# Optimization experiments

Hardware: AMD Instinct MI355X
Metric: run time of the kernel (lower is better)

The kernel has to match this reference:

```python
import jax, jax.numpy as jnp
import numpy as np

N = 50000
E = 600000


def gcn_conv(x, W, b, src, dst, n):
    # PyG GCNConv: h = x @ W; add self-loops; symmetric normalization; aggregate; + bias
    h = x @ W  # [N, out]
    deg = jnp.zeros((n,), h.dtype).at[dst].add(1.0) + 1.0  # self-loop included
    dinv = jax.lax.rsqrt(deg)  # deg >= 1, always finite
    coef = dinv[src] * dinv[dst]  # [E]
    msg = h[src] * coef[:, None]  # [E, out]  (the memory-bound gather)
    agg = jax.ops.segment_sum(msg, dst, num_segments=n)
    agg = agg + h * (dinv * dinv)[:, None]  # self-loop contribution
    return agg + b


def setup_inputs() -> dict:
    key = jax.random.key(0)
    ks = jax.random.split(key, 8)
    x = jax.random.normal(ks[0], (N, 128), dtype=jnp.float32)
    edge_index = jax.random.randint(ks[1], (2, E), 0, N, dtype=jnp.int64 if jax.config.jax_enable_x64 else jnp.int32)
    def glorot(k, fan_in, fan_out):
        s = jnp.sqrt(6.0 / (fan_in + fan_out))
        return jax.random.uniform(k, (fan_in, fan_out), jnp.float32, -s, s)
    W1 = glorot(ks[2], 128, 128)
    b1 = jnp.zeros((128,), jnp.float32)
    W2 = glorot(ks[3], 128, 64)
    b2 = jnp.zeros((64,), jnp.float32)
    W3 = glorot(ks[4], 64, 16)
    b3 = jnp.zeros((16,), jnp.float32)
    return {"x": x, "edge_index": edge_index, "W1": W1, "b1": b1, "W2": W2, "b2": b2, "W3": W3, "b3": b3}


def reference(x, edge_index, W1, b1, W2, b2, W3, b3):
    src, dst = edge_index[0], edge_index[1]
    n = x.shape[0]
    h = jax.nn.relu(gcn_conv(x, W1, b1, src, dst, n))
    h = jax.nn.relu(gcn_conv(h, W2, b2, src, dst, n))
    h = gcn_conv(h, W3, b3, src, dst, n)
    return h
```

## Files before the change

### kernel.cpp

```cpp
#include <hip/hip_runtime.h>
#include <hip/hip_fp16.h>
#include <type_traits>


typedef _Float16 f16x8 __attribute__((ext_vector_type(8)));
typedef float f32x4 __attribute__((ext_vector_type(4)));

#define CSR_CAP 64

__device__ inline float2 h2f(unsigned int u) {
  __half2 h = __builtin_bit_cast(__half2, u);
  return __half22float2(h);
}

__device__ inline void fma8h(float4& a0, float4& a1, const uint4& g, float w) {
  float2 f0 = h2f(g.x), f1 = h2f(g.y), f2 = h2f(g.z), f3 = h2f(g.w);
  a0.x = fmaf(f0.x, w, a0.x);
  a0.y = fmaf(f0.y, w, a0.y);
  a0.z = fmaf(f1.x, w, a0.z);
  a0.w = fmaf(f1.y, w, a0.w);
  a1.x = fmaf(f2.x, w, a1.x);
  a1.y = fmaf(f2.y, w, a1.y);
  a1.z = fmaf(f3.x, w, a1.z);
  a1.w = fmaf(f3.y, w, a1.w);
}

__device__ inline unsigned int pack2h(float x, float y) {
  __half2 h = __floats2half2_rn(x, y);
  return __builtin_bit_cast(unsigned int, h);
}

__device__ inline uint2 pack4h(const float4& v) {
  uint2 r;
  r.x = pack2h(v.x, v.y);
  r.y = pack2h(v.z, v.w);
  return r;
}

template <int K, int F, typename TIN>
__global__ __launch_bounds__(256) void gemm_mfma(const TIN* __restrict__ A,
                                                 const float* __restrict__ W,
                                                 __half* __restrict__ C16, int n,
                                                 int nwaves, int ngemm,
                                                 const int* __restrict__ src,
                                                 const int* __restrict__ dst,
                                                 int* __restrict__ cur,
                                                 int* __restrict__ csr, int E) {
  constexpr int KP = K + 8;
  constexpr int KS = K / 32;
  constexpr int NT = F / 16;

  if (blockIdx.x >= ngemm) {
    int e = (blockIdx.x - ngemm) * 256 + threadIdx.x;
    if (e < E) {
      int d = dst[e];
      int pos = atomicAdd(&cur[d], 1);
      if (pos >= CSR_CAP) pos = CSR_CAP - 1;
      csr[(size_t)d * CSR_CAP + pos] = src[e];
    }
    return;
  }

  __shared__ __half Ws[F * KP];

  int t = threadIdx.x;
  for (int i = t; i < K * F; i += 256) {
    int kk = i / F, nn = i % F;
    Ws[nn * KP + kk] = __float2half(W[i]);
  }
  __syncthreads();

  int wave = blockIdx.x * 4 + (t >> 6);
  if (wave >= nwaves) return;
  int lane = t & 63;
  int m = lane & 15;
  int quad = lane >> 4;

  int arow = wave * 16 + m;
  if (arow >= n) arow = n - 1;

  f16x8 af[KS];
  if constexpr (std::is_same_v<TIN, float>) {
#pragma unroll
    for (int ks = 0; ks < KS; ++ks) {
      const float* p = A + (size_t)arow * K + ks * 32 + quad * 8;
      float4 lo = *(const float4*)p;
      float4 hi = *(const float4*)(p + 4);
      f16x8 a;
      a[0] = (_Float16)lo.x; a[1] = (_Float16)lo.y;
      a[2] = (_Float16)lo.z; a[3] = (_Float16)lo.w;
      a[4] = (_Float16)hi.x; a[5] = (_Float16)hi.y;
      a[6] = (_Float16)hi.z; a[7] = (_Float16)hi.w;
      af[ks] = a;
    }
  } else {
#pragma unroll
    for (int ks = 0; ks < KS; ++ks)
      af[ks] = *(const f16x8*)(const void*)&A[(size_t)arow * K + ks * 32 + quad * 8];
  }

  f32x4 acc[NT];
#pragma unroll
  for (int nt = 0; nt < NT; ++nt) acc[nt] = (f32x4){0.f, 0.f, 0.f, 0.f};
#pragma unroll
  for (int nt = 0; nt < NT; ++nt)
#pragma unroll
    for (int ks = 0; ks < KS; ++ks) {
      f16x8 b = *(const f16x8*)(const void*)&Ws[(nt * 16 + m) * KP + ks * 32 + quad * 8];
      acc[nt] = __builtin_amdgcn_mfma_f32_16x16x32_f16(af[ks], b, acc[nt], 0, 0, 0);
    }

  int rbase = wave * 16 + quad * 4;
#pragma unroll
  for (int nt = 0; nt < NT; ++nt)
#pragma unroll
    for (int r = 0; r < 4; ++r) {
      int rr = rbase + r;
      if (rr < n) C16[(size_t)rr * F + nt * 16 + m] = __float2half(acc[nt][r]);
    }
}

template <int K, int F, int CPL, int EU>
__global__ __launch_bounds__(512) void aggmm(
    const __half* __restrict__ hprev, const float* __restrict__ W,
    const float* __restrict__ bias, const int* __restrict__ cnt,
    const int* __restrict__ csr, __half* __restrict__ C16, int n) {
  constexpr int KP = K + 8;
  constexpr int KS = K / 32;
  constexpr int NT = F / 16;
  constexpr int TPN = 8;
  constexpr int RS = K / 8;
  static_assert(TPN * CPL == RS, "chunk coverage");

  __shared__ __half Ws[F * KP];
  __shared__ __half As[64 * KP];

  int t = threadIdx.x;
  for (int i = t; i < K * F; i += 512) {
    int kk = i / F, nn = i % F;
    Ws[nn * KP + kk] = __float2half(W[i]);
  }

  int wid = t >> 6;
  int lane = t & 63;
  int nb = blockIdx.x * 64;

  {
    int sub = lane / TPN;
    int fl = lane % TPN;
    int nib = wid * 8 + sub;
    int node = nb + nib;
    int nd = node < n ? node : n - 1;
    const uint4* h4 = (const uint4*)hprev;
    int c0 = cnt[nd];
    float di = rsqrtf((float)c0 + 1.0f);
    float sc = di * di;
    int cc = c0 < CSR_CAP ? c0 : CSR_CAP;
    float4 acc[CPL][2];
#pragma unroll
    for (int c = 0; c < CPL; ++c) {
      acc[c][0] = make_float4(0.f, 0.f, 0.f, 0.f);
      acc[c][1] = make_float4(0.f, 0.f, 0.f, 0.f);
    }
#pragma unroll
    for (int c = 0; c < CPL; ++c) {
      uint4 sv = h4[(size_t)nd * RS + fl + c * TPN];
      fma8h(acc[c][0], acc[c][1], sv, sc);
    }
    int j = nd * CSR_CAP;
    int e = j + cc;
    int p[EU];
#pragma unroll
    for (int u = 0; u < EU; ++u) p[u] = csr[j + u];
    for (; j + EU <= e;) {
      uint4 g[EU][CPL];
#pragma unroll
      for (int u = 0; u < EU; ++u)
#pragma unroll
        for (int c = 0; c < CPL; ++c) g[u][c] = h4[(size_t)p[u] * RS + fl + c * TPN];
      int cs[EU];
#pragma unroll
      for (int u = 0; u < EU; ++u) cs[u] = cnt[p[u]];
      j += EU;
      int pn[EU];
#pragma unroll
      for (int u = 0; u < EU; ++u) pn[u] = csr[j + u];
#pragma unroll
      for (int u = 0; u < EU; ++u) {
        float w = rsqrtf((float)cs[u] + 1.0f) * di;
#pragma unroll
        for (int c = 0; c < CPL; ++c) fma8h(acc[c][0], acc[c][1], g[u][c], w);
      }
#pragma unroll
      for (int u = 0; u < EU; ++u) p[u] = pn[u];
    }
#pragma unroll
    for (int u = 0; u < EU; ++u) {
      if (j + u < e) {
        float w = rsqrtf((float)cnt[p[u]] + 1.0f) * di;
#pragma unroll
        for (int c = 0; c < CPL; ++c) {
          uint4 g = h4[(size_t)p[u] * RS + fl + c * TPN];
          fma8h(acc[c][0], acc[c][1], g, w);
        }
      }
    }
#pragma unroll
    for (int c = 0; c < CPL; ++c) {
      int ch = fl + c * TPN;
      float4 b0 = *(const float4*)&bias[ch * 8];
      float4 b1 = *(const float4*)&bias[ch * 8 + 4];
      float4 r0 = make_float4(fmaxf(acc[c][0].x + b0.x, 0.f), fmaxf(acc[c][0].y + b0.y, 0.f),
                              fmaxf(acc[c][0].z + b0.z, 0.f), fmaxf(acc[c][0].w + b0.w, 0.f));
      float4 r1 = make_float4(fmaxf(acc[c][1].x + b1.x, 0.f), fmaxf(acc[c][1].y + b1.y, 0.f),
                              fmaxf(acc[c][1].z + b1.z, 0.f), fmaxf(acc[c][1].w + b1.w, 0.f));
      uint2 lo = pack4h(r0), hi = pack4h(r1);
      uint4 pk;
      pk.x = lo.x; pk.y = lo.y; pk.z = hi.x; pk.w = hi.y;
      *(uint4*)&As[(size_t)nib * KP + ch * 8] = pk;
    }
  }

  __syncthreads();

  if (wid < 4) {
    int m = lane & 15;
    int quad = lane >> 4;
    const __half* At = &As[(size_t)wid * 16 * KP];
    f16x8 af[KS];
#pragma unroll
    for (int ks = 0; ks < KS; ++ks)
      af[ks] = *(const f16x8*)(const void*)&At[m * KP + ks * 32 + quad * 8];

    f32x4 acc2[NT];
#pragma unroll
    for (int nt = 0; nt < NT; ++nt) acc2[nt] = (f32x4){0.f, 0.f, 0.f, 0.f};
#pragma unroll
    for (int nt = 0; nt < NT; ++nt)
#pragma unroll
      for (int ks = 0; ks < KS; ++ks) {
        f16x8 bfr = *(const f16x8*)(const void*)&Ws[(nt * 16 + m) * KP + ks * 32 + quad * 8];
        acc2[nt] = __builtin_amdgcn_mfma_f32_16x16x32_f16(af[ks], bfr, acc2[nt], 0, 0, 0);
      }

    int rbase = nb + wid * 16 + quad * 4;
#pragma unroll
    for (int nt = 0; nt < NT; ++nt)
#pragma unroll
      for (int r = 0; r < 4; ++r) {
        int rr = rbase + r;
        if (rr < n) C16[(size_t)rr * F + nt * 16 + m] = __float2half(acc2[nt][r]);
      }
  }
}

__global__ __launch_bounds__(256) void agg_final(
    const __half* __restrict__ h16, const int* __restrict__ cnt,
    const int* __restrict__ csr, const float* __restrict__ bias,
    float* __restrict__ out, int n) {
  int node = blockIdx.x * 64 + threadIdx.x / 4;
  int q = threadIdx.x & 3;
  int half = q >> 1;
  int fl = q & 1;
  bool valid = node < n;
  int nd = valid ? node : n - 1;

  const uint4* h4 = (const uint4*)h16;
  int c0 = cnt[nd];
  float di = rsqrtf((float)c0 + 1.0f);
  int cc = c0 < CSR_CAP ? c0 : CSR_CAP;
  float4 a0 = make_float4(0.f, 0.f, 0.f, 0.f);
  float4 a1 = make_float4(0.f, 0.f, 0.f, 0.f);
  if (half == 0) {
    uint4 sv = h4[(size_t)nd * 2 + fl];
    fma8h(a0, a1, sv, di * di);
  }
  int s = nd * CSR_CAP;
  int e = s + cc;
  int j = s + half;
  for (; j + 2 < e; j += 4) {
    int p0 = csr[j];
    int p1 = csr[j + 2];
    int ca = cnt[p0];
    int cb = cnt[p1];
    uint4 g0 = h4[(size_t)p0 * 2 + fl];
    uint4 g1 = h4[(size_t)p1 * 2 + fl];
    fma8h(a0, a1, g0, rsqrtf((float)ca + 1.0f) * di);
    fma8h(a0, a1, g1, rsqrtf((float)cb + 1.0f) * di);
  }
  for (; j < e; j += 2) {
    int p = csr[j];
    uint4 g = h4[(size_t)p * 2 + fl];
    fma8h(a0, a1, g, rsqrtf((float)cnt[p] + 1.0f) * di);
  }

  a0.x += __shfl_xor(a0.x, 2);
  a0.y += __shfl_xor(a0.y, 2);
  a0.z += __shfl_xor(a0.z, 2);
  a0.w += __shfl_xor(a0.w, 2);
  a1.x += __shfl_xor(a1.x, 2);
  a1.y += __shfl_xor(a1.y, 2);
  a1.z += __shfl_xor(a1.z, 2);
  a1.w += __shfl_xor(a1.w, 2);

  if (valid && half == 0) {
    float4 b0 = *(const float4*)&bias[fl * 8];
    float4 b1 = *(const float4*)&bias[fl * 8 + 4];
    float4 r0 = make_float4(a0.x + b0.x, a0.y + b0.y, a0.z + b0.z, a0.w + b0.w);
    float4 r1 = make_float4(a1.x + b1.x, a1.y + b1.y, a1.z + b1.z, a1.w + b1.w);
    float* op = &out[(size_t)node * 16 + fl * 8];
    *(float4*)op = r0;
    *(float4*)(op + 4) = r1;
  }
}


extern "C" void kernel_launch(void* const* d_in, const int* in_sizes, int n_in,
                              void* d_out, int out_size, void* d_ws, size_t ws_size,
                              hipStream_t stream) {
  const float* x = (const float*)d_in[0];
  const int* edge = (const int*)d_in[1];
  const float* W1 = (const float*)d_in[2];
  const float* b1 = (const float*)d_in[3];
  const float* W2 = (const float*)d_in[4];
  const float* b2 = (const float*)d_in[5];
  const float* W3 = (const float*)d_in[6];
  const float* b3 = (const float*)d_in[7];

  const int N = in_sizes[0] / 128;
  const int E = in_sizes[1] / 2;
  const int* src = edge;
  const int* dstp = edge + E;
  float* out = (float*)d_out;

  size_t off = 0;
  auto take = [&](size_t bytes) -> void* {
    void* r = (char*)d_ws + off;
    off += (bytes + 255) & ~(size_t)255;
    return r;
  };
  int* cur = (int*)take((size_t)N * 4);
  int* csr = (int*)take((size_t)N * CSR_CAP * 4 + 256);
  __half* t1 = (__half*)take((size_t)N * 128 * 2);
  __half* t2 = (__half*)take((size_t)N * 64 * 2);
  __half* t3 = (__half*)take((size_t)N * 16 * 2);

  hipMemsetAsync(d_ws, 0, ((size_t)N * 4 + 255) & ~(size_t)255, stream);

  int nwaves = (N + 15) / 16;
  int gblk = (nwaves + 3) / 4;
  int fblk = (N + 63) / 64;
  int eg = (E + 255) / 256;

  gemm_mfma<128, 128, float><<<gblk + eg, 256, 0, stream>>>(x, W1, t1, N, nwaves, gblk,
                                                            src, dstp, cur, csr, E);

  aggmm<128, 64, 2, 4><<<fblk, 512, 0, stream>>>(t1, W2, b1, cur, csr, t2, N);
  aggmm<64, 16, 1, 4><<<fblk, 512, 0, stream>>>(t2, W3, b2, cur, csr, t3, N);
  agg_final<<<fblk, 256, 0, stream>>>(t3, cur, csr, b3, out, N);
}
```

Baseline: 181.1 us.

## Co-locate CSR build in extra waves of GEMM blocks with unrolled atomics

Instead of launching separate blocks for CSR construction after the GEMM blocks, each GEMM block now has 512 threads. The upper 256 threads run a grid-stride CSR insertion loop, unrolled by 4 so several dst/src loads and atomics are in flight at once. This aims to overlap the atomic-bound edge scatter with the MFMA GEMM on the same CUs and to cut the block count. The cost is that raising launch bounds to 512 tightens the register budget for the GEMM path, and the barrier behaviour depends on the early-exit waves matching the single __syncthreads.

```diff
diff --git a/kernel.cpp b/kernel.cpp
--- a/kernel.cpp
+++ b/kernel.cpp
@@ -38,10 +38,10 @@
 }
 
 template <int K, int F, typename TIN>
-__global__ __launch_bounds__(256) void gemm_mfma(const TIN* __restrict__ A,
+__global__ __launch_bounds__(512) void gemm_mfma(const TIN* __restrict__ A,
                                                  const float* __restrict__ W,
                                                  __half* __restrict__ C16, int n,
-                                                 int nwaves, int ngemm,
+                                                 int nwaves,
                                                  const int* __restrict__ src,
                                                  const int* __restrict__ dst,
                                                  int* __restrict__ cur,
@@ -50,20 +50,39 @@
   constexpr int KS = K / 32;
   constexpr int NT = F / 16;
 
-  if (blockIdx.x >= ngemm) {
-    int e = (blockIdx.x - ngemm) * 256 + threadIdx.x;
-    if (e < E) {
-      int d = dst[e];
-      int pos = atomicAdd(&cur[d], 1);
-      if (pos >= CSR_CAP) pos = CSR_CAP - 1;
-      csr[(size_t)d * CSR_CAP + pos] = src[e];
+  __shared__ __half Ws[F * KP];
+
+  int t = threadIdx.x;
+
+  if (t >= 256) {
+    __syncthreads();
+    int base = blockIdx.x * 256 + (t - 256);
+    int stride = gridDim.x * 256;
+    for (int e0 = base; e0 < E; e0 += 4 * stride) {
+      int d[4], s[4];
+      bool v[4];
+#pragma unroll
+      for (int u = 0; u < 4; ++u) {
+        int e = e0 + u * stride;
+        v[u] = e < E;
+        int ee = v[u] ? e : 0;
+        d[u] = dst[ee];
+        s[u] = src[ee];
+      }
+      int pos[4];
+#pragma unroll
+      for (int u = 0; u < 4; ++u)
+        if (v[u]) pos[u] = atomicAdd(&cur[d[u]], 1);
+#pragma unroll
+      for (int u = 0; u < 4; ++u)
+        if (v[u]) {
+          int p = pos[u] >= CSR_CAP ? CSR_CAP - 1 : pos[u];
+          csr[(size_t)d[u] * CSR_CAP + p] = s[u];
+        }
     }
     return;
   }
 
-  __shared__ __half Ws[F * KP];
-
-  int t = threadIdx.x;
   for (int i = t; i < K * F; i += 256) {
     int kk = i / F, nn = i % F;
     Ws[nn * KP + kk] = __float2half(W[i]);
@@ -350,10 +369,9 @@
   int nwaves = (N + 15) / 16;
   int gblk = (nwaves + 3) / 4;
   int fblk = (N + 63) / 64;
-  int eg = (E + 255) / 256;
-
-  gemm_mfma<128, 128, float><<<gblk + eg, 256, 0, stream>>>(x, W1, t1, N, nwaves, gblk,
-                                                            src, dstp, cur, csr, E);
+
+  gemm_mfma<128, 128, float><<<gblk, 512, 0, stream>>>(x, W1, t1, N, nwaves,
+                                                       src, dstp, cur, csr, E);
 
   aggmm<128, 64, 2, 4><<<fblk, 512, 0, stream>>>(t1, W2, b1, cur, csr, t2, N);
   aggmm<64, 16, 1, 4><<<fblk, 512, 0, stream>>>(t2, W3, b2, cur, csr, t3, N);
```

After: 171.7 us (median of 2 runs). 5.2% less time.
